# Performance work log

Measured on AMD Instinct MI355X. Metric: run time of the kernel, lower is better.

Reference implementation:

```python
import jax, jax.numpy as jnp
import numpy as np

ALPHA = 1.0   # alpha=1 -> loss = alpha*loss_shape; temporal term weighted by (1-alpha)=0
GAMMA = 0.01  # soft-DTW smoothing
G = 0.05      # logistic weight steepness (weighted-DTW, Jeong et al. 2011)
BIG = 1e9     # finite 'infinity' (keeps vjp NaN-free vs. true inf)


def _softdtw(D, gamma):
    # Soft-DTW value of cost matrix D [N,N] via anti-diagonal (wavefront) scan.
    # R(i,j) = D[i,j] + softmin_gamma(R(i-1,j-1), R(i-1,j), R(i,j-1)),
    # R(-1,-1)=0, other out-of-range = +inf. Diagonal k holds cells (i, k-i).
    N = D.shape[-1]
    i = jnp.arange(N)

    def step(carry, k):
        r2, r1 = carry            # diagonals k-2 and k-1, indexed by row i
        j = k - i
        valid = (j >= 0) & (j < N)
        dk = jnp.where(valid, D[i, jnp.clip(j, 0, N - 1)], 0.0)
        up = jnp.where(i > 0, jnp.roll(r1, 1), BIG)     # R(i-1, j)
        left = r1                                        # R(i, j-1) (BIG where invalid)
        dg = jnp.where(i > 0, jnp.roll(r2, 1), BIG)      # R(i-1, j-1)
        dg = jnp.where((i == 0) & (j == 0), 0.0, dg)     # R(-1,-1) = 0 boundary
        smin = -gamma * jax.nn.logsumexp(jnp.stack([-dg, -up, -left]) / gamma, axis=0)
        rk = jnp.where(valid, dk + smin, BIG)
        return (r1, rk), None

    r0 = jnp.full((N,), BIG, dtype=D.dtype)
    (_, rlast), _ = jax.lax.scan(step, (r0, r0), jnp.arange(2 * N - 1))
    return rlast[N - 1]  # cell (N-1, N-1)


def _weighted_dilate(inp, tgt):
    B, N, _ = inp.shape
    idx = jnp.arange(N, dtype=inp.dtype)
    # modified-logistic weight on |i-j|, midpoint N/2, steepness g
    w = 1.0 / (1.0 + jnp.exp(-G * (jnp.abs(idx[:, None] - idx[None, :]) - N / 2.0)))
    # pairwise squared euclidean cost: D[b,i,j] = sum_d (tgt[b,i,d]-inp[b,j,d])^2
    D = jnp.sum((tgt[:, :, None, :] - inp[:, None, :, :]) ** 2, axis=-1) * w
    sdtw = jax.vmap(lambda d: _softdtw(d, GAMMA))(D)  # [B]
    loss_shape = jnp.mean(sdtw)
    return ALPHA * loss_shape  # (1-alpha)*loss_temporal == 0 at default alpha=1


def setup_inputs() -> dict:
    key = jax.random.key(0)
    k1, k2 = jax.random.split(key)
    B, N, Dm = 32, 1024, 1
    return {
        "input": jax.random.normal(k1, (B, N, Dm), dtype=jnp.float32),
        "target": jax.random.normal(k2, (B, N, Dm), dtype=jnp.float32),
    }


def reference(input, target):
    return _weighted_dilate(input, target)
```

## Files before the change

kernel.cpp:

```cpp
#include <hip/hip_runtime.h>
#include <math.h>

#define NN 1024
#define BATCH 32
#define P 8
#define NW 4
#define THREADS 256
#define DD 32
#define SW 32
#define SPAN 160
#define NT 64
#define RB 4
#define GW 0.05f
#define K2 144.2695040888963f
#define INV_K2 0.0069314718055994531f
#define BIGS 1.4426950408889634e11f

#define EXP2F(x) __builtin_amdgcn_exp2f(x)
#define LOG2F(x) __builtin_amdgcn_logf(x)

union F2U { float2 f; unsigned long long u; };

__device__ __forceinline__ float dppshr(float oldv, float src) {
    return __int_as_float(__builtin_amdgcn_update_dpp(
        __float_as_int(oldv), __float_as_int(src), 0x138, 0xF, 0xF, false));
}

__global__ __launch_bounds__(THREADS) void sdtw_pipe8(
        const float* __restrict__ inp, const float* __restrict__ tgt,
        float* __restrict__ out, int* __restrict__ flags,
        int* __restrict__ acks, unsigned long long* __restrict__ gx)
{
    __shared__ float xs[NN];
    __shared__ float wlblk[3136];
    __shared__ float2 exch[2][SPAN];

    const int bid = blockIdx.x;
    const int b = bid & 31;
    const int p = bid >> 5;
    const int tid = threadIdx.x;
    const int w = tid >> 6;
    const int lane = tid & 63;

    for (int tdx = tid; tdx < NN; tdx += THREADS) {
        xs[tdx] = inp[b * NN + tdx];
        float mO = (float)(2 * tdx + 1) - 1023.0f;
        float mE = (float)(2 * tdx) - 1023.0f;
        wlblk[544 + tdx]        = K2 / (1.0f + __expf(-GW * (fabsf(mO) - 512.0f)));
        wlblk[544 + 1024 + tdx] = K2 / (1.0f + __expf(-GW * (fabsf(mE) - 512.0f)));
    }

    const int i = 128 * p - (DD - 1) + SW * w + lane;
    const int i0 = i - lane;
    const bool rowValid = (unsigned)i < (unsigned)NN;
    int ic = min(max(i, 0), NN - 1);
    const float ti = tgt[b * NN + ic];
    const int imask = rowValid ? i : 0x3FFFFFFF;
    const float* wpBase = &wlblk[544 + 511 - i];

    float m1 = BIGS, s1 = 1.0f, m2 = BIGS, s2 = 1.0f;
    float mdgp = (i == 0) ? 0.0f : BIGS;
    float sdgp = 1.0f;
    float bndUpM = BIGS, bndUpS = 1.0f;
    float xv = 0.0f;
    int ackC = 0;

    __syncthreads();

    const int fin = b * P + p;
    const int fout = fin + 1;
    unsigned long long* gout = gx + (size_t)fout * RB * DD;
    const unsigned long long* ginb = gx + (size_t)fin * RB * DD;

    for (int t = 0; t < NT; ++t) {
        if (w == NW - 1 && p < P - 1 && t >= RB && ackC <= t - RB) {
            ackC = __hip_atomic_load(&acks[fout], __ATOMIC_RELAXED,
                                     __HIP_MEMORY_SCOPE_AGENT);
        }

        const int kbase = t << 5;
        const float* wp = wpBase + (t << 4);
        int c = kbase - 1 - i;  c = min(max(c, 0), NN - 1);
        xv = xs[c];
        int c0 = kbase - i0;    c0 = min(max(c0, 0), NN - 1);
        const float xf0 = xs[c0];
        const int jj0 = kbase - imask;

        #pragma unroll
        for (int d = 0; d < DD; ++d) {
            xv = dppshr((d == 0) ? xf0 : xv, xv);
            const float mUp = dppshr((d == 0) ? bndUpM : m1, m1);
            const float sUp = dppshr((d == 0) ? bndUpS : s1, s1);
            const float mDg = mdgp, sDg = sdgp;
            const float mLf = m1,  sLf = s1;
            const float wv = (d & 1) ? wp[1024 + ((d + 1) >> 1)] : wp[(d >> 1)];
            const float diff = ti - xv;
            const float dk = diff * diff * wv;
            const float M = fminf(fminf(mDg, mUp), mLf);
            const float eDg = EXP2F(M - mDg);
            const float eUp = EXP2F(M - mUp);
            const float eLf = EXP2F(M - mLf);
            const float sN = sDg * eDg + sUp * eUp + sLf * eLf;
            float mN = dk + M;
            mN = (jj0 >= -d) ? mN : BIGS;
            m2 = m1; s2 = s1;
            m1 = mN; s1 = sN;
            mdgp = mUp; sdgp = sUp;
        }
        if (t == NT - 1) break;

        m1 -= LOG2F(s1);     s1 = 1.0f;
        m2 -= LOG2F(s2);     s2 = 1.0f;
        mdgp -= LOG2F(sdgp); sdgp = 1.0f;
        bndUpS = 1.0f;

        const int buf = t & 1;
        if (lane >= DD - 1) exch[buf][SW * w + lane] = make_float2(m1, m2);
        if (w == NW - 1 && p < P - 1) {
            if (t >= RB) {
                while (ackC < t - (RB - 1)) {
                    __builtin_amdgcn_s_sleep(1);
                    ackC = __hip_atomic_load(&acks[fout], __ATOMIC_RELAXED,
                                             __HIP_MEMORY_SCOPE_AGENT);
                }
            }
            if (lane >= DD - 1 && lane < 63) {
                F2U v; v.f = make_float2(m1, m2);
                __hip_atomic_store(&gout[(size_t)(t & (RB - 1)) * DD + (lane - (DD - 1))],
                                   v.u, __ATOMIC_RELAXED, __HIP_MEMORY_SCOPE_AGENT);
            }
            asm volatile("s_waitcnt vmcnt(0)" ::: "memory");
            if (lane == 63)
                __hip_atomic_store(&flags[fout], t + 1, __ATOMIC_RELAXED,
                                   __HIP_MEMORY_SCOPE_AGENT);
        }
        __syncthreads();
        if (w > 0) {
            if (lane < DD - 1) { float2 v = exch[buf][SW * w + lane]; m1 = v.x; m2 = v.y; }
            float2 bv = exch[buf][SW * w - 1];
            float nd = dppshr(0.0f, m2);
            if (lane == 0)           { bndUpM = bv.x; mdgp = bv.y; }
            else if (lane <= DD - 2) mdgp = nd;
        } else if (p > 0) {
            int fl;
            do {
                fl = __hip_atomic_load(&flags[fin], __ATOMIC_RELAXED,
                                       __HIP_MEMORY_SCOPE_AGENT);
                if (fl < t + 1) __builtin_amdgcn_s_sleep(1);
            } while (fl < t + 1);
            asm volatile("" ::: "memory");
            const unsigned long long* gslot = ginb + (size_t)(t & (RB - 1)) * DD;
            if (lane < DD - 1) {
                F2U v; v.u = __hip_atomic_load((unsigned long long*)&gslot[lane + 1],
                                               __ATOMIC_RELAXED, __HIP_MEMORY_SCOPE_AGENT);
                m1 = v.f.x; m2 = v.f.y;
            }
            F2U bv; bv.f = make_float2(BIGS, BIGS);
            if (lane == 0)
                bv.u = __hip_atomic_load((unsigned long long*)&gslot[0],
                                         __ATOMIC_RELAXED, __HIP_MEMORY_SCOPE_AGENT);
            float nd = dppshr(0.0f, m2);
            if (lane == 0)           { bndUpM = bv.f.x; mdgp = bv.f.y; }
            else if (lane <= DD - 2) mdgp = nd;
            asm volatile("s_waitcnt vmcnt(0)" ::: "memory");
            if (lane == 0)
                __hip_atomic_store(&acks[fin], t + 1, __ATOMIC_RELAXED,
                                   __HIP_MEMORY_SCOPE_AGENT);
        } else {
            bndUpM = BIGS;
        }
    }

    if (i == NN - 1)
        atomicAdd(out, (m2 - LOG2F(s2)) * (INV_K2 / (float)BATCH));
}

extern "C" void kernel_launch(void* const* d_in, const int* in_sizes, int n_in,
                              void* d_out, int out_size, void* d_ws, size_t ws_size,
                              hipStream_t stream) {
    const float* inp = (const float*)d_in[0];
    const float* tgt = (const float*)d_in[1];
    float* out = (float*)d_out;

    int* flags = (int*)d_ws;
    int* acks  = (int*)((char*)d_ws + 1024);
    unsigned long long* gx = (unsigned long long*)((char*)d_ws + 2048);

    hipMemsetAsync(d_out, 0, sizeof(float), stream);
    sdtw_pipe8<<<BATCH * P, THREADS, 0, stream>>>(inp, tgt, out, flags, acks, gx);
}
```

Before: 226.7 us.

## Interleave two batch elements per block to hide wavefront dependency latency

New measurement: 284.3 us. +25.4%, slower.

```diff
diff --git a/kernel.cpp b/kernel.cpp
--- a/kernel.cpp
+++ b/kernel.cpp
@@ -3,6 +3,7 @@
 
 #define NN 1024
 #define BATCH 32
+#define NPAIR 16
 #define P 8
 #define NW 4
 #define THREADS 256
@@ -26,24 +27,26 @@
         __float_as_int(oldv), __float_as_int(src), 0x138, 0xF, 0xF, false));
 }
 
-__global__ __launch_bounds__(THREADS) void sdtw_pipe8(
+__global__ __launch_bounds__(THREADS) void sdtw_pair(
         const float* __restrict__ inp, const float* __restrict__ tgt,
         float* __restrict__ out, int* __restrict__ flags,
         int* __restrict__ acks, unsigned long long* __restrict__ gx)
 {
-    __shared__ float xs[NN];
+    __shared__ float xsA[NN], xsB[NN];
     __shared__ float wlblk[3136];
-    __shared__ float2 exch[2][SPAN];
+    __shared__ float4 exch[2][SPAN];
 
     const int bid = blockIdx.x;
-    const int b = bid & 31;
-    const int p = bid >> 5;
+    const int q = bid & 15;
+    const int p = bid >> 4;
+    const int bA = q, bB = q + NPAIR;
     const int tid = threadIdx.x;
     const int w = tid >> 6;
     const int lane = tid & 63;
 
     for (int tdx = tid; tdx < NN; tdx += THREADS) {
-        xs[tdx] = inp[b * NN + tdx];
+        xsA[tdx] = inp[bA * NN + tdx];
+        xsB[tdx] = inp[bB * NN + tdx];
         float mO = (float)(2 * tdx + 1) - 1023.0f;
         float mE = (float)(2 * tdx) - 1023.0f;
         wlblk[544 + tdx]        = K2 / (1.0f + __expf(-GW * (fabsf(mO) - 512.0f)));
@@ -54,23 +57,25 @@
     const int i0 = i - lane;
     const bool rowValid = (unsigned)i < (unsigned)NN;
     int ic = min(max(i, 0), NN - 1);
-    const float ti = tgt[b * NN + ic];
+    const float tiA = tgt[bA * NN + ic];
+    const float tiB = tgt[bB * NN + ic];
     const int imask = rowValid ? i : 0x3FFFFFFF;
     const float* wpBase = &wlblk[544 + 511 - i];
 
-    float m1 = BIGS, s1 = 1.0f, m2 = BIGS, s2 = 1.0f;
-    float mdgp = (i == 0) ? 0.0f : BIGS;
-    float sdgp = 1.0f;
-    float bndUpM = BIGS, bndUpS = 1.0f;
-    float xv = 0.0f;
+    float m1A = BIGS, s1A = 1.0f, m2A = BIGS, s2A = 1.0f;
+    float m1B = BIGS, s1B = 1.0f, m2B = BIGS, s2B = 1.0f;
+    float mdgpA = (i == 0) ? 0.0f : BIGS, sdgpA = 1.0f;
+    float mdgpB = mdgpA, sdgpB = 1.0f;
+    float bndUpMA = BIGS, bndUpMB = BIGS;
+    float xvA = 0.0f, xvB = 0.0f;
     int ackC = 0;
 
     __syncthreads();
 
-    const int fin = b * P + p;
+    const int fin = q * P + p;
     const int fout = fin + 1;
-    unsigned long long* gout = gx + (size_t)fout * RB * DD;
-    const unsigned long long* ginb = gx + (size_t)fin * RB * DD;
+    unsigned long long* gout = gx + (size_t)fout * RB * DD * 2;
+    const unsigned long long* ginb = gx + (size_t)fin * RB * DD * 2;
 
     for (int t = 0; t < NT; ++t) {
         if (w == NW - 1 && p < P - 1 && t >= RB && ackC <= t - RB) {
@@ -81,41 +86,62 @@
         const int kbase = t << 5;
         const float* wp = wpBase + (t << 4);
         int c = kbase - 1 - i;  c = min(max(c, 0), NN - 1);
-        xv = xs[c];
+        xvA = xsA[c]; xvB = xsB[c];
         int c0 = kbase - i0;    c0 = min(max(c0, 0), NN - 1);
-        const float xf0 = xs[c0];
+        const float xf0A = xsA[c0], xf0B = xsB[c0];
         const int jj0 = kbase - imask;
 
         #pragma unroll
         for (int d = 0; d < DD; ++d) {
-            xv = dppshr((d == 0) ? xf0 : xv, xv);
-            const float mUp = dppshr((d == 0) ? bndUpM : m1, m1);
-            const float sUp = dppshr((d == 0) ? bndUpS : s1, s1);
-            const float mDg = mdgp, sDg = sdgp;
-            const float mLf = m1,  sLf = s1;
             const float wv = (d & 1) ? wp[1024 + ((d + 1) >> 1)] : wp[(d >> 1)];
-            const float diff = ti - xv;
-            const float dk = diff * diff * wv;
-            const float M = fminf(fminf(mDg, mUp), mLf);
-            const float eDg = EXP2F(M - mDg);
-            const float eUp = EXP2F(M - mUp);
-            const float eLf = EXP2F(M - mLf);
-            const float sN = sDg * eDg + sUp * eUp + sLf * eLf;
-            float mN = dk + M;
-            mN = (jj0 >= -d) ? mN : BIGS;
-            m2 = m1; s2 = s1;
-            m1 = mN; s1 = sN;
-            mdgp = mUp; sdgp = sUp;
+            const bool vmask = (jj0 >= -d);
+            xvA = dppshr((d == 0) ? xf0A : xvA, xvA);
+            {
+                const float mUp = dppshr((d == 0) ? bndUpMA : m1A, m1A);
+                const float sUp = dppshr((d == 0) ? 1.0f : s1A, s1A);
+                const float mDg = mdgpA, sDg = sdgpA;
+                const float mLf = m1A,  sLf = s1A;
+                const float diff = tiA - xvA;
+                const float dk = diff * diff * wv;
+                const float M = fminf(fminf(mDg, mUp), mLf);
+                const float eDg = EXP2F(M - mDg);
+                const float eUp = EXP2F(M - mUp);
+                const float eLf = EXP2F(M - mLf);
+                const float sN = sDg * eDg + sUp * eUp + sLf * eLf;
+                float mN = dk + M;
+                mN = vmask ? mN : BIGS;
+                m2A = m1A; s2A = s1A; m1A = mN; s1A = sN;
+                mdgpA = mUp; sdgpA = sUp;
+            }
+            xvB = dppshr((d == 0) ? xf0B : xvB, xvB);
+            {
+                const float mUp = dppshr((d == 0) ? bndUpMB : m1B, m1B);
+                const float sUp = dppshr((d == 0) ? 1.0f : s1B, s1B);
+                const float mDg = mdgpB, sDg = sdgpB;
+                const float mLf = m1B,  sLf = s1B;
+                const float diff = tiB - xvB;
+                const float dk = diff * diff * wv;
+                const float M = fminf(fminf(mDg, mUp), mLf);
+                const float eDg = EXP2F(M - mDg);
+                const float eUp = EXP2F(M - mUp);
+                const float eLf = EXP2F(M - mLf);
+                const float sN = sDg * eDg + sUp * eUp + sLf * eLf;
+                float mN = dk + M;
+                mN = vmask ? mN : BIGS;
+                m2B = m1B; s2B = s1B; m1B = mN; s1B = sN;
+                mdgpB = mUp; sdgpB = sUp;
+            }
         }
         if (t == NT - 1) break;
 
-        m1 -= LOG2F(s1);     s1 = 1.0f;
-        m2 -= LOG2F(s2);     s2 = 1.0f;
-        mdgp -= LOG2F(sdgp); sdgp = 1.0f;
-        bndUpS = 1.0f;
+        m1A -= LOG2F(s1A); s1A = 1.0f;   m1B -= LOG2F(s1B); s1B = 1.0f;
+        m2A -= LOG2F(s2A); s2A = 1.0f;   m2B -= LOG2F(s2B); s2B = 1.0f;
+        mdgpA -= LOG2F(sdgpA); sdgpA = 1.0f;
+        mdgpB -= LOG2F(sdgpB); sdgpB = 1.0f;
 
         const int buf = t & 1;
-        if (lane >= DD - 1) exch[buf][SW * w + lane] = make_float2(m1, m2);
+        if (lane >= DD - 1)
+            exch[buf][SW * w + lane] = make_float4(m1A, m2A, m1B, m2B);
         if (w == NW - 1 && p < P - 1) {
             if (t >= RB) {
                 while (ackC < t - (RB - 1)) {
@@ -125,9 +151,15 @@
                 }
             }
             if (lane >= DD - 1 && lane < 63) {
-                F2U v; v.f = make_float2(m1, m2);
-                __hip_atomic_store(&gout[(size_t)(t & (RB - 1)) * DD + (lane - (DD - 1))],
-                                   v.u, __ATOMIC_RELAXED, __HIP_MEMORY_SCOPE_AGENT);
+                const int row = lane - (DD - 1);
+                unsigned long long* dst =
+                    gout + (size_t)(t & (RB - 1)) * DD * 2 + row * 2;
+                F2U a; a.f = make_float2(m1A, m2A);
+                F2U bv; bv.f = make_float2(m1B, m2B);
+                __hip_atomic_store(&dst[0], a.u, __ATOMIC_RELAXED,
+                                   __HIP_MEMORY_SCOPE_AGENT);
+                __hip_atomic_store(&dst[1], bv.u, __ATOMIC_RELAXED,
+                                   __HIP_MEMORY_SCOPE_AGENT);
             }
             asm volatile("s_waitcnt vmcnt(0)" ::: "memory");
             if (lane == 63)
@@ -136,11 +168,16 @@
         }
         __syncthreads();
         if (w > 0) {
-            if (lane < DD - 1) { float2 v = exch[buf][SW * w + lane]; m1 = v.x; m2 = v.y; }
-            float2 bv = exch[buf][SW * w - 1];
-            float nd = dppshr(0.0f, m2);
-            if (lane == 0)           { bndUpM = bv.x; mdgp = bv.y; }
-            else if (lane <= DD - 2) mdgp = nd;
+            if (lane < DD - 1) {
+                float4 v = exch[buf][SW * w + lane];
+                m1A = v.x; m2A = v.y; m1B = v.z; m2B = v.w;
+            }
+            float4 bv = exch[buf][SW * w - 1];
+            float ndA = dppshr(0.0f, m2A);
+            float ndB = dppshr(0.0f, m2B);
+            if (lane == 0) {
+                bndUpMA = bv.x; mdgpA = bv.y; bndUpMB = bv.z; mdgpB = bv.w;
+            } else if (lane <= DD - 2) { mdgpA = ndA; mdgpB = ndB; }
         } else if (p > 0) {
             int fl;
             do {
@@ -149,30 +186,41 @@
                 if (fl < t + 1) __builtin_amdgcn_s_sleep(1);
             } while (fl < t + 1);
             asm volatile("" ::: "memory");
-            const unsigned long long* gslot = ginb + (size_t)(t & (RB - 1)) * DD;
+            const unsigned long long* gslot = ginb + (size_t)(t & (RB - 1)) * DD * 2;
             if (lane < DD - 1) {
-                F2U v; v.u = __hip_atomic_load((unsigned long long*)&gslot[lane + 1],
-                                               __ATOMIC_RELAXED, __HIP_MEMORY_SCOPE_AGENT);
-                m1 = v.f.x; m2 = v.f.y;
-            }
-            F2U bv; bv.f = make_float2(BIGS, BIGS);
-            if (lane == 0)
-                bv.u = __hip_atomic_load((unsigned long long*)&gslot[0],
-                                         __ATOMIC_RELAXED, __HIP_MEMORY_SCOPE_AGENT);
-            float nd = dppshr(0.0f, m2);
-            if (lane == 0)           { bndUpM = bv.f.x; mdgp = bv.f.y; }
-            else if (lane <= DD - 2) mdgp = nd;
+                F2U a, bv;
+                a.u  = __hip_atomic_load((unsigned long long*)&gslot[(lane + 1) * 2],
+                                         __ATOMIC_RELAXED, __HIP_MEMORY_SCOPE_AGENT);
+                bv.u = __hip_atomic_load((unsigned long long*)&gslot[(lane + 1) * 2 + 1],
+                                         __ATOMIC_RELAXED, __HIP_MEMORY_SCOPE_AGENT);
+                m1A = a.f.x; m2A = a.f.y; m1B = bv.f.x; m2B = bv.f.y;
+            }
+            F2U ba, bb; ba.f = make_float2(BIGS, BIGS); bb.f = make_float2(BIGS, BIGS);
+            if (lane == 0) {
+                ba.u = __hip_atomic_load((unsigned long long*)&gslot[0],
+                                         __ATOMIC_RELAXED, __HIP_MEMORY_SCOPE_AGENT);
+                bb.u = __hip_atomic_load((unsigned long long*)&gslot[1],
+                                         __ATOMIC_RELAXED, __HIP_MEMORY_SCOPE_AGENT);
+            }
+            float ndA = dppshr(0.0f, m2A);
+            float ndB = dppshr(0.0f, m2B);
+            if (lane == 0) {
+                bndUpMA = ba.f.x; mdgpA = ba.f.y; bndUpMB = bb.f.x; mdgpB = bb.f.y;
+            } else if (lane <= DD - 2) { mdgpA = ndA; mdgpB = ndB; }
             asm volatile("s_waitcnt vmcnt(0)" ::: "memory");
             if (lane == 0)
                 __hip_atomic_store(&acks[fin], t + 1, __ATOMIC_RELAXED,
                                    __HIP_MEMORY_SCOPE_AGENT);
         } else {
-            bndUpM = BIGS;
+            bndUpMA = BIGS; bndUpMB = BIGS;
         }
     }
 
-    if (i == NN - 1)
-        atomicAdd(out, (m2 - LOG2F(s2)) * (INV_K2 / (float)BATCH));
+    if (i == NN - 1) {
+        float rA = m2A - LOG2F(s2A);
+        float rB = m2B - LOG2F(s2B);
+        atomicAdd(out, (rA + rB) * (INV_K2 / (float)BATCH));
+    }
 }
 
 extern "C" void kernel_launch(void* const* d_in, const int* in_sizes, int n_in,
@@ -187,5 +235,5 @@
     unsigned long long* gx = (unsigned long long*)((char*)d_ws + 2048);
 
     hipMemsetAsync(d_out, 0, sizeof(float), stream);
-    sdtw_pipe8<<<BATCH * P, THREADS, 0, stream>>>(inp, tgt, out, flags, acks, gx);
+    sdtw_pair<<<NPAIR * P, THREADS, 0, stream>>>(inp, tgt, out, flags, acks, gx);
 }
```

## Replace block barrier with per-wave LDS flag ring and prefetch inter-block boundary

Applied to the files above, without the earlier changes.

Result: slower. 240.8 us (+6.2%).

```diff
diff --git a/kernel.cpp b/kernel.cpp
--- a/kernel.cpp
+++ b/kernel.cpp
@@ -8,7 +8,6 @@
 #define THREADS 256
 #define DD 32
 #define SW 32
-#define SPAN 160
 #define NT 64
 #define RB 4
 #define GW 0.05f
@@ -26,14 +25,16 @@
         __float_as_int(oldv), __float_as_int(src), 0x138, 0xF, 0xF, false));
 }
 
-__global__ __launch_bounds__(THREADS) void sdtw_pipe8(
+__global__ __launch_bounds__(THREADS) void sdtw_flow(
         const float* __restrict__ inp, const float* __restrict__ tgt,
         float* __restrict__ out, int* __restrict__ flags,
         int* __restrict__ acks, unsigned long long* __restrict__ gx)
 {
     __shared__ float xs[NN];
     __shared__ float wlblk[3136];
-    __shared__ float2 exch[2][SPAN];
+    __shared__ float2 lring[NW - 1][RB][DD];
+    __shared__ int lflag[NW - 1];
+    __shared__ int lack[NW - 1];
 
     const int bid = blockIdx.x;
     const int b = bid & 31;
@@ -49,6 +50,7 @@
         wlblk[544 + tdx]        = K2 / (1.0f + __expf(-GW * (fabsf(mO) - 512.0f)));
         wlblk[544 + 1024 + tdx] = K2 / (1.0f + __expf(-GW * (fabsf(mE) - 512.0f)));
     }
+    if (tid < NW - 1) { lflag[tid] = 0; lack[tid] = 0; }
 
     const int i = 128 * p - (DD - 1) + SW * w + lane;
     const int i0 = i - lane;
@@ -61,21 +63,49 @@
     float m1 = BIGS, s1 = 1.0f, m2 = BIGS, s2 = 1.0f;
     float mdgp = (i == 0) ? 0.0f : BIGS;
     float sdgp = 1.0f;
-    float bndUpM = BIGS, bndUpS = 1.0f;
+    float bndUpM = BIGS;
     float xv = 0.0f;
     int ackC = 0;
 
     __syncthreads();
+
+    const bool inGlb  = (w == 0 && p > 0);
+    const bool inLds  = (w > 0);
+    const bool outGlb = (w == NW - 1 && p < P - 1);
+    const bool outLds = (w < NW - 1);
 
     const int fin = b * P + p;
     const int fout = fin + 1;
     unsigned long long* gout = gx + (size_t)fout * RB * DD;
     const unsigned long long* ginb = gx + (size_t)fin * RB * DD;
 
+    float2 pfE = make_float2(BIGS, BIGS);
+    float2 pfB = make_float2(BIGS, BIGS);
+
     for (int t = 0; t < NT; ++t) {
-        if (w == NW - 1 && p < P - 1 && t >= RB && ackC <= t - RB) {
+        if (outGlb && t >= RB && ackC <= t - RB) {
             ackC = __hip_atomic_load(&acks[fout], __ATOMIC_RELAXED,
                                      __HIP_MEMORY_SCOPE_AGENT);
+        }
+        if (inGlb && t < NT - 1) {
+            int fl;
+            do {
+                fl = __hip_atomic_load(&flags[fin], __ATOMIC_RELAXED,
+                                       __HIP_MEMORY_SCOPE_AGENT);
+                if (fl < t + 1) __builtin_amdgcn_s_sleep(1);
+            } while (fl < t + 1);
+            asm volatile("" ::: "memory");
+            const unsigned long long* gslot = ginb + (size_t)(t & (RB - 1)) * DD;
+            if (lane < DD - 1) {
+                F2U v; v.u = __hip_atomic_load((unsigned long long*)&gslot[lane + 1],
+                                               __ATOMIC_RELAXED, __HIP_MEMORY_SCOPE_AGENT);
+                pfE = v.f;
+            }
+            if (lane == 0) {
+                F2U v; v.u = __hip_atomic_load((unsigned long long*)&gslot[0],
+                                               __ATOMIC_RELAXED, __HIP_MEMORY_SCOPE_AGENT);
+                pfB = v.f;
+            }
         }
 
         const int kbase = t << 5;
@@ -90,7 +120,7 @@
         for (int d = 0; d < DD; ++d) {
             xv = dppshr((d == 0) ? xf0 : xv, xv);
             const float mUp = dppshr((d == 0) ? bndUpM : m1, m1);
-            const float sUp = dppshr((d == 0) ? bndUpS : s1, s1);
+            const float sUp = dppshr((d == 0) ? 1.0f : s1, s1);
             const float mDg = mdgp, sDg = sdgp;
             const float mLf = m1,  sLf = s1;
             const float wv = (d & 1) ? wp[1024 + ((d + 1) >> 1)] : wp[(d >> 1)];
@@ -103,20 +133,30 @@
             const float sN = sDg * eDg + sUp * eUp + sLf * eLf;
             float mN = dk + M;
             mN = (jj0 >= -d) ? mN : BIGS;
-            m2 = m1; s2 = s1;
-            m1 = mN; s1 = sN;
+            m2 = m1; s2 = s1; m1 = mN; s1 = sN;
             mdgp = mUp; sdgp = sUp;
         }
         if (t == NT - 1) break;
 
-        m1 -= LOG2F(s1);     s1 = 1.0f;
-        m2 -= LOG2F(s2);     s2 = 1.0f;
+        m1 -= LOG2F(s1); s1 = 1.0f;
+        m2 -= LOG2F(s2); s2 = 1.0f;
         mdgp -= LOG2F(sdgp); sdgp = 1.0f;
-        bndUpS = 1.0f;
-
-        const int buf = t & 1;
-        if (lane >= DD - 1) exch[buf][SW * w + lane] = make_float2(m1, m2);
-        if (w == NW - 1 && p < P - 1) {
+
+        const int slot = t & (RB - 1);
+
+        if (outLds) {
+            if (t >= RB) {
+                while (__hip_atomic_load(&lack[w], __ATOMIC_RELAXED,
+                                         __HIP_MEMORY_SCOPE_WORKGROUP) < t - (RB - 1))
+                    __builtin_amdgcn_s_sleep(1);
+            }
+            if (lane >= DD - 1 && lane < 63)
+                lring[w][slot][lane - (DD - 1)] = make_float2(m1, m2);
+            if (lane == 0)
+                __hip_atomic_store(&lflag[w], t + 1, __ATOMIC_RELEASE,
+                                   __HIP_MEMORY_SCOPE_WORKGROUP);
+        }
+        if (outGlb) {
             if (t >= RB) {
                 while (ackC < t - (RB - 1)) {
                     __builtin_amdgcn_s_sleep(1);
@@ -126,7 +166,7 @@
             }
             if (lane >= DD - 1 && lane < 63) {
                 F2U v; v.f = make_float2(m1, m2);
-                __hip_atomic_store(&gout[(size_t)(t & (RB - 1)) * DD + (lane - (DD - 1))],
+                __hip_atomic_store(&gout[(size_t)slot * DD + (lane - (DD - 1))],
                                    v.u, __ATOMIC_RELAXED, __HIP_MEMORY_SCOPE_AGENT);
             }
             asm volatile("s_waitcnt vmcnt(0)" ::: "memory");
@@ -134,33 +174,25 @@
                 __hip_atomic_store(&flags[fout], t + 1, __ATOMIC_RELAXED,
                                    __HIP_MEMORY_SCOPE_AGENT);
         }
-        __syncthreads();
-        if (w > 0) {
-            if (lane < DD - 1) { float2 v = exch[buf][SW * w + lane]; m1 = v.x; m2 = v.y; }
-            float2 bv = exch[buf][SW * w - 1];
+
+        if (inLds) {
+            while (__hip_atomic_load(&lflag[w - 1], __ATOMIC_ACQUIRE,
+                                     __HIP_MEMORY_SCOPE_WORKGROUP) < t + 1)
+                __builtin_amdgcn_s_sleep(1);
+            float2 e = make_float2(0.0f, 0.0f);
+            if (lane < DD - 1) e = lring[w - 1][slot][lane + 1];
+            float2 bv = lring[w - 1][slot][0];
+            if (lane == 0)
+                __hip_atomic_store(&lack[w - 1], t + 1, __ATOMIC_RELEASE,
+                                   __HIP_MEMORY_SCOPE_WORKGROUP);
+            if (lane < DD - 1) { m1 = e.x; m2 = e.y; }
             float nd = dppshr(0.0f, m2);
             if (lane == 0)           { bndUpM = bv.x; mdgp = bv.y; }
             else if (lane <= DD - 2) mdgp = nd;
-        } else if (p > 0) {
-            int fl;
-            do {
-                fl = __hip_atomic_load(&flags[fin], __ATOMIC_RELAXED,
-                                       __HIP_MEMORY_SCOPE_AGENT);
-                if (fl < t + 1) __builtin_amdgcn_s_sleep(1);
-            } while (fl < t + 1);
-            asm volatile("" ::: "memory");
-            const unsigned long long* gslot = ginb + (size_t)(t & (RB - 1)) * DD;
-            if (lane < DD - 1) {
-                F2U v; v.u = __hip_atomic_load((unsigned long long*)&gslot[lane + 1],
-                                               __ATOMIC_RELAXED, __HIP_MEMORY_SCOPE_AGENT);
-                m1 = v.f.x; m2 = v.f.y;
-            }
-            F2U bv; bv.f = make_float2(BIGS, BIGS);
-            if (lane == 0)
-                bv.u = __hip_atomic_load((unsigned long long*)&gslot[0],
-                                         __ATOMIC_RELAXED, __HIP_MEMORY_SCOPE_AGENT);
+        } else if (inGlb) {
+            if (lane < DD - 1) { m1 = pfE.x; m2 = pfE.y; }
             float nd = dppshr(0.0f, m2);
-            if (lane == 0)           { bndUpM = bv.f.x; mdgp = bv.f.y; }
+            if (lane == 0)           { bndUpM = pfB.x; mdgp = pfB.y; }
             else if (lane <= DD - 2) mdgp = nd;
             asm volatile("s_waitcnt vmcnt(0)" ::: "memory");
             if (lane == 0)
@@ -187,5 +219,5 @@
     unsigned long long* gx = (unsigned long long*)((char*)d_ws + 2048);
 
     hipMemsetAsync(d_out, 0, sizeof(float), stream);
-    sdtw_pipe8<<<BATCH * P, THREADS, 0, stream>>>(inp, tgt, out, flags, acks, gx);
+    sdtw_flow<<<BATCH * P, THREADS, 0, stream>>>(inp, tgt, out, flags, acks, gx);
 }
```
